# Kernel optimization log

Hardware: AMD Instinct MI355X
Metric: run time of the kernel (lower is better)

The kernel has to match this reference:

```python
import jax, jax.numpy as jnp
import numpy as np

B, C, H, W = 8, 64, 256, 256  # H must equal W for the second matmul


def setup_inputs() -> dict:
    key = jax.random.key(0)
    kq, kk, kv = jax.random.split(key, 3)
    Q = jax.random.normal(kq, (B, C, H, W), dtype=jnp.float32)
    K = jax.random.normal(kk, (B, C, H, W), dtype=jnp.float32)
    V = jax.random.normal(kv, (B, C, H, W), dtype=jnp.float32)
    di = jnp.ones((1,), dtype=jnp.float32)  # learned scalar scale
    return {"Q": Q, "K": K, "V": V, "di": di}


def reference(Q, K, V, di):
    # similarity[b,c,i,k] = sum_w Q[b,c,i,w] * K[b,c,k,w], scaled by di
    sim = jnp.einsum('bciw,bckw->bcik', Q, K) * di[0]
    attn = jax.nn.softmax(sim, axis=-1)  # [B,C,H,H]
    # residual = attn @ V^T -> [B,C,H,H]; output is residual^T:
    # out[b,c,i,j] = sum_k attn[b,c,j,k] * V[b,c,i,k]
    out = jnp.einsum('bcjk,bcik->bcij', attn, V)
    return out
```

## Files before the change

### kernel.cpp

```cpp
#include <hip/hip_runtime.h>
#include <hip/hip_bf16.h>


typedef __attribute__((ext_vector_type(8))) _Float16 f16x8;
typedef __attribute__((ext_vector_type(4))) float f32x4;
typedef __attribute__((ext_vector_type(16))) float f32x16;

#define BARRIER() asm volatile("s_waitcnt lgkmcnt(0)\n\ts_barrier" ::: "memory")

__device__ __forceinline__ f32x4 mfma16h(f16x8 a, f16x8 b, f32x4 c) {
  return __builtin_amdgcn_mfma_f32_16x16x32_f16(a, b, c, 0, 0, 0);
}
__device__ __forceinline__ f32x16 mfma32h(f16x8 a, f16x8 b, f32x16 c) {
  return __builtin_amdgcn_mfma_f32_32x32x16_f16(a, b, c, 0, 0, 0);
}
__device__ __forceinline__ f16x8 cvt8(f32x4 a, f32x4 b) {
  f16x8 r;
  r[0] = (_Float16)a[0]; r[1] = (_Float16)a[1];
  r[2] = (_Float16)a[2]; r[3] = (_Float16)a[3];
  r[4] = (_Float16)b[0]; r[5] = (_Float16)b[1];
  r[6] = (_Float16)b[2]; r[7] = (_Float16)b[3];
  return r;
}
__device__ __forceinline__ int swzA(int row, int byteCol) {
  return row * 512 + (byteCol ^ ((row & 15) << 4));
}
__device__ __forceinline__ int swzV(int row, int byteCol) {
  return row * 256 + (byteCol ^ ((row & 15) << 4));
}

__global__ __launch_bounds__(1024, 4) void attn_fused15(
    const float* __restrict__ Q, const float* __restrict__ K,
    const float* __restrict__ V, const float* __restrict__ di,
    float* __restrict__ out) {
  __shared__ short Kbuf[2][32 * 256];
  __shared__ short Abuf[256 * 256];
  short* Vlds0 = &Kbuf[0][0];
  short* Vlds1 = &Kbuf[1][0];

  const int t = threadIdx.x;
  const int lane = t & 63;
  const int wv = t >> 6;
  const int l15 = lane & 15;
  const int l4 = (lane >> 4) & 3;
  const int l31 = lane & 31;
  const int h5 = lane >> 5;

  const int bc = blockIdx.x;

  const float dival = di[0];
  const size_t base = (size_t)bc << 16;
  const float* Qs = Q + base;
  const float* Ks = K + base;
  const float* Vs = V + base;
  float* Os = out + base;

  const int sr = t >> 5;
  const int scf = (t & 31) << 3;

  f32x4 kpA0, kpA1, kpB0, kpB1;
  {
    const float* p = Ks + sr * 256 + scf;
    kpA0 = *(const f32x4*)p;
    kpA1 = *(const f32x4*)(p + 4);
    kpB0 = *(const f32x4*)(p + 8192);
    kpB1 = *(const f32x4*)(p + 8192 + 4);
  }
  f16x8 qh[8];
  {
    const float* qrow = Qs + (size_t)(16 * wv + l15) * 256 + 8 * l4;
#pragma unroll
    for (int s = 0; s < 8; ++s)
      qh[s] = cvt8(*(const f32x4*)(qrow + 32 * s),
                   *(const f32x4*)(qrow + 32 * s + 4));
  }

  f32x4 acc[16];
#pragma unroll
  for (int i = 0; i < 16; ++i) acc[i] = (f32x4){0.f, 0.f, 0.f, 0.f};

#pragma unroll
  for (int ch = 0; ch < 8; ++ch) {
    short* kb = Kbuf[ch & 1];
    if ((ch & 1) == 0) {
      *(f16x8*)((char*)kb + swzA(sr, scf * 2)) = cvt8(kpA0, kpA1);
    } else {
      *(f16x8*)((char*)kb + swzA(sr, scf * 2)) = cvt8(kpB0, kpB1);
    }
    BARRIER();
    if (ch < 6) {
      const float* p = Ks + (ch + 2) * 8192 + sr * 256 + scf;
      if ((ch & 1) == 0) {
        kpA0 = *(const f32x4*)p;
        kpA1 = *(const f32x4*)(p + 4);
      } else {
        kpB0 = *(const f32x4*)p;
        kpB1 = *(const f32x4*)(p + 4);
      }
    }
    __builtin_amdgcn_s_setprio(1);
#pragma unroll
    for (int kf = 0; kf < 2; ++kf) {
      const int kr = 16 * kf + l15;
      f32x4 a = acc[2 * ch + kf];
#pragma unroll
      for (int s = 0; s < 8; ++s) {
        f16x8 bh =
            *(const f16x8*)((const char*)kb + swzA(kr, 64 * s + 16 * l4));
        a = mfma16h(qh[s], bh, a);
      }
      acc[2 * ch + kf] = a;
    }
    __builtin_amdgcn_s_setprio(0);
  }

  const int vr = t >> 4;
  const int vcf = (t & 15) * 8;
  f32x4 vpA[2], vpB[2];
  {
    const float* p = Vs + (size_t)vr * 256 + vcf;
    vpA[0] = *(const f32x4*)p;
    vpA[1] = *(const f32x4*)(p + 4);
    const float* q = p + 128;
    vpB[0] = *(const f32x4*)q;
    vpB[1] = *(const f32x4*)(q + 4);
  }

  float mx[4] = {-1e30f, -1e30f, -1e30f, -1e30f};
#pragma unroll
  for (int idx = 0; idx < 16; ++idx)
#pragma unroll
    for (int r = 0; r < 4; ++r) {
      acc[idx][r] *= dival;
      mx[r] = fmaxf(mx[r], acc[idx][r]);
    }
#pragma unroll
  for (int o = 1; o <= 8; o <<= 1)
#pragma unroll
    for (int r = 0; r < 4; ++r) mx[r] = fmaxf(mx[r], __shfl_xor(mx[r], o));
  float sm[4] = {0.f, 0.f, 0.f, 0.f};
#pragma unroll
  for (int idx = 0; idx < 16; ++idx)
#pragma unroll
    for (int r = 0; r < 4; ++r) {
      acc[idx][r] = __expf(acc[idx][r] - mx[r]);
      sm[r] += acc[idx][r];
    }
#pragma unroll
  for (int o = 1; o <= 8; o <<= 1)
#pragma unroll
    for (int r = 0; r < 4; ++r) sm[r] += __shfl_xor(sm[r], o);
#pragma unroll
  for (int r = 0; r < 4; ++r) sm[r] = 1.0f / sm[r];
#pragma unroll
  for (int idx = 0; idx < 16; ++idx)
#pragma unroll
    for (int r = 0; r < 4; ++r) {
      const int row = 16 * wv + 4 * l4 + r;
      *(_Float16*)((char*)Abuf + swzA(row, 2 * (16 * idx + l15))) =
          (_Float16)(acc[idx][r] * sm[r]);
    }
  BARRIER();

  const int ig = wv & 1;
  const int jg = wv >> 1;
  f16x8 pb[16];
#pragma unroll
  for (int kx = 0; kx < 16; ++kx)
    pb[kx] =
        *(const f16x8*)((const char*)Abuf + swzA(32 * jg + l31, 32 * kx + 16 * h5));

  f32x16 o = {};
#pragma unroll
  for (int cc = 0; cc < 8; ++cc) {
    const int kh = cc & 1;
    short* vb = (cc & 1) ? Vlds1 : Vlds0;
    if ((cc & 1) == 0) {
      *(f16x8*)((char*)vb + swzV(vr, 2 * vcf)) = cvt8(vpA[0], vpA[1]);
    } else {
      *(f16x8*)((char*)vb + swzV(vr, 2 * vcf)) = cvt8(vpB[0], vpB[1]);
    }
    BARRIER();
    if (cc < 6) {
      const float* p = Vs + (size_t)(64 * ((cc + 2) >> 1) + vr) * 256 +
                       ((cc & 1) ? 128 : 0) + vcf;
      if ((cc & 1) == 0) {
        vpA[0] = *(const f32x4*)p;
        vpA[1] = *(const f32x4*)(p + 4);
      } else {
        vpB[0] = *(const f32x4*)p;
        vpB[1] = *(const f32x4*)(p + 4);
      }
    }
    __builtin_amdgcn_s_setprio(1);
#pragma unroll
    for (int kk = 0; kk < 8; ++kk) {
      f16x8 vfrag = *(const f16x8*)((const char*)vb +
                                    swzV(32 * ig + l31, 32 * kk + 16 * h5));
      o = mfma32h(vfrag, pb[8 * kh + kk], o);
    }
    __builtin_amdgcn_s_setprio(0);
    if (kh == 1) {
      const int rbase = 64 * (cc >> 1) + 32 * ig + 4 * h5;
      const int col = 32 * jg + l31;
#pragma unroll
      for (int reg = 0; reg < 16; ++reg) {
        const int rw = (reg & 3) + 8 * (reg >> 2);
        Os[(size_t)(rbase + rw) * 256 + col] = o[reg];
      }
      o = (f32x16){};
    }
  }
}

extern "C" void kernel_launch(void* const* d_in, const int* in_sizes, int n_in,
                              void* d_out, int out_size, void* d_ws,
                              size_t ws_size, hipStream_t stream) {
  const float* Q = (const float*)d_in[0];
  const float* K = (const float*)d_in[1];
  const float* V = (const float*)d_in[2];
  const float* di = (const float*)d_in[3];
  float* out = (float*)d_out;
  const int BC = in_sizes[0] / (256 * 256);
  hipLaunchKernelGGL(attn_fused15, dim3(BC), dim3(1024), 0, stream, Q, K, V,
                     di, out);
}
```

Measured before the change: 105.3 us.

## Restructure second matmul into 64x64 per-wave tiles with K-chunked V staging

The attn·V stage now gives each wave a 64x64 output tile held in four 32x32 MFMA accumulators. It iterates over the reduction dimension in four chunks of 64 V columns, staged into a single LDS buffer with a narrower swizzle. Previously each wave computed 32x32 tiles over 64-row V chunks and preloaded attention fragments into registers. The new scheme reuses each loaded fragment across two MFMAs, cutting LDS reads per MFMA, and writes output once at the end. In exchange it adds an extra barrier per chunk because the V buffer is single-buffered, which loses the previous load/compute overlap, and it raises accumulator register pressure.

```diff
diff --git a/kernel.cpp b/kernel.cpp
--- a/kernel.cpp
+++ b/kernel.cpp
@@ -26,17 +26,16 @@
   return row * 512 + (byteCol ^ ((row & 15) << 4));
 }
 __device__ __forceinline__ int swzV(int row, int byteCol) {
-  return row * 256 + (byteCol ^ ((row & 15) << 4));
-}
-
-__global__ __launch_bounds__(1024, 4) void attn_fused15(
+  return row * 128 + (byteCol ^ ((row & 7) << 4));
+}
+
+__global__ __launch_bounds__(1024, 4) void attn_fused17(
     const float* __restrict__ Q, const float* __restrict__ K,
     const float* __restrict__ V, const float* __restrict__ di,
     float* __restrict__ out) {
   __shared__ short Kbuf[2][32 * 256];
   __shared__ short Abuf[256 * 256];
-  short* Vlds0 = &Kbuf[0][0];
-  short* Vlds1 = &Kbuf[1][0];
+  short* Vlds = &Kbuf[0][0];
 
   const int t = threadIdx.x;
   const int lane = t & 63;
@@ -114,16 +113,13 @@
     __builtin_amdgcn_s_setprio(0);
   }
 
-  const int vr = t >> 4;
-  const int vcf = (t & 15) * 8;
-  f32x4 vpA[2], vpB[2];
+  const int vr = t >> 2;
+  const int vq = (t & 3) << 4;
+  f32x4 vp[4];
   {
-    const float* p = Vs + (size_t)vr * 256 + vcf;
-    vpA[0] = *(const f32x4*)p;
-    vpA[1] = *(const f32x4*)(p + 4);
-    const float* q = p + 128;
-    vpB[0] = *(const f32x4*)q;
-    vpB[1] = *(const f32x4*)(q + 4);
+    const float* p = Vs + (size_t)vr * 256 + vq;
+#pragma unroll
+    for (int e = 0; e < 4; ++e) vp[e] = *(const f32x4*)(p + 4 * e);
   }
 
   float mx[4] = {-1e30f, -1e30f, -1e30f, -1e30f};
@@ -162,54 +158,50 @@
     }
   BARRIER();
 
-  const int ig = wv & 1;
-  const int jg = wv >> 1;
-  f16x8 pb[16];
-#pragma unroll
-  for (int kx = 0; kx < 16; ++kx)
-    pb[kx] =
-        *(const f16x8*)((const char*)Abuf + swzA(32 * jg + l31, 32 * kx + 16 * h5));
-
-  f32x16 o = {};
-#pragma unroll
-  for (int cc = 0; cc < 8; ++cc) {
-    const int kh = cc & 1;
-    short* vb = (cc & 1) ? Vlds1 : Vlds0;
-    if ((cc & 1) == 0) {
-      *(f16x8*)((char*)vb + swzV(vr, 2 * vcf)) = cvt8(vpA[0], vpA[1]);
-    } else {
-      *(f16x8*)((char*)vb + swzV(vr, 2 * vcf)) = cvt8(vpB[0], vpB[1]);
-    }
+  const int ig = wv & 3;
+  const int jg = wv >> 2;
+  f32x16 o00 = {}, o01 = {}, o10 = {}, o11 = {};
+#pragma unroll
+  for (int kc = 0; kc < 4; ++kc) {
+    *(f16x8*)((char*)Vlds + swzV(vr, 2 * vq)) = cvt8(vp[0], vp[1]);
+    *(f16x8*)((char*)Vlds + swzV(vr, 2 * vq + 16)) = cvt8(vp[2], vp[3]);
     BARRIER();
-    if (cc < 6) {
-      const float* p = Vs + (size_t)(64 * ((cc + 2) >> 1) + vr) * 256 +
-                       ((cc & 1) ? 128 : 0) + vcf;
-      if ((cc & 1) == 0) {
-        vpA[0] = *(const f32x4*)p;
-        vpA[1] = *(const f32x4*)(p + 4);
-      } else {
-        vpB[0] = *(const f32x4*)p;
-        vpB[1] = *(const f32x4*)(p + 4);
-      }
+    if (kc < 3) {
+      const float* p = Vs + (size_t)vr * 256 + (kc + 1) * 64 + vq;
+#pragma unroll
+      for (int e = 0; e < 4; ++e) vp[e] = *(const f32x4*)(p + 4 * e);
     }
     __builtin_amdgcn_s_setprio(1);
 #pragma unroll
-    for (int kk = 0; kk < 8; ++kk) {
-      f16x8 vfrag = *(const f16x8*)((const char*)vb +
-                                    swzV(32 * ig + l31, 32 * kk + 16 * h5));
-      o = mfma32h(vfrag, pb[8 * kh + kk], o);
+    for (int kk = 0; kk < 4; ++kk) {
+      const int vCol = 32 * kk + 16 * h5;
+      f16x8 va0 =
+          *(const f16x8*)((const char*)Vlds + swzV(64 * ig + l31, vCol));
+      f16x8 va1 =
+          *(const f16x8*)((const char*)Vlds + swzV(64 * ig + 32 + l31, vCol));
+      const int aCol = 128 * kc + 32 * kk + 16 * h5;
+      f16x8 pb0 =
+          *(const f16x8*)((const char*)Abuf + swzA(64 * jg + l31, aCol));
+      f16x8 pb1 =
+          *(const f16x8*)((const char*)Abuf + swzA(64 * jg + 32 + l31, aCol));
+      o00 = mfma32h(va0, pb0, o00);
+      o01 = mfma32h(va0, pb1, o01);
+      o10 = mfma32h(va1, pb0, o10);
+      o11 = mfma32h(va1, pb1, o11);
     }
     __builtin_amdgcn_s_setprio(0);
-    if (kh == 1) {
-      const int rbase = 64 * (cc >> 1) + 32 * ig + 4 * h5;
-      const int col = 32 * jg + l31;
-#pragma unroll
-      for (int reg = 0; reg < 16; ++reg) {
-        const int rw = (reg & 3) + 8 * (reg >> 2);
-        Os[(size_t)(rbase + rw) * 256 + col] = o[reg];
-      }
-      o = (f32x16){};
-    }
+    if (kc < 3) BARRIER();
+  }
+
+  const int rb = 64 * ig + 4 * h5;
+  const int cb = 64 * jg + l31;
+#pragma unroll
+  for (int reg = 0; reg < 16; ++reg) {
+    const int rw = (reg & 3) + 8 * (reg >> 2);
+    Os[(size_t)(rb + rw) * 256 + cb] = o00[reg];
+    Os[(size_t)(rb + rw) * 256 + cb + 32] = o01[reg];
+    Os[(size_t)(rb + 32 + rw) * 256 + cb] = o10[reg];
+    Os[(size_t)(rb + 32 + rw) * 256 + cb + 32] = o11[reg];
   }
 }
 
@@ -222,6 +214,6 @@
   const float* di = (const float*)d_in[3];
   float* out = (float*)d_out;
   const int BC = in_sizes[0] / (256 * 256);
-  hipLaunchKernelGGL(attn_fused15, dim3(BC), dim3(1024), 0, stream, Q, K, V,
+  hipLaunchKernelGGL(attn_fused17, dim3(BC), dim3(1024), 0, stream, Q, K, V,
                      di, out);
 }
```

After: 114.9 us. 1.09x slower.
